# Performance work log

Hardware: AMD Instinct MI355X
Metric: run time of the kernel (lower is better)

Reference implementation:

```python
import math
import jax, jax.numpy as jnp
import numpy as np

B, S, HID = 2, 1024, 4096
NH, NKV, HD = 32, 8, 128
G = NH // NKV            # query heads per KV head (GQA group size)
PAST = 1024              # tokens already in the cache per sequence
L = PAST + S             # total KV tokens attended per sequence
SLOTS = 16384            # paged KV-cache slots (flat token addressing)
MAXPOS = 8192
THETA = 10000.0


def _rope_table():
    inv_freq = 1.0 / (THETA ** (np.arange(0, HD, 2, dtype=np.float64) / HD))
    freqs = np.arange(MAXPOS, dtype=np.float64)[:, None] * inv_freq[None, :]
    emb = np.concatenate([freqs, freqs], axis=-1)          # [MAXPOS, HD]
    return jnp.asarray(np.stack([np.cos(emb), np.sin(emb)], axis=1), jnp.float32)  # [MAXPOS,2,HD]


def setup_inputs() -> dict:
    key = jax.random.key(0)
    ks = jax.random.split(key, 6)
    hidden_states = jax.random.normal(ks[0], (B, S, HID), jnp.float32)
    kv_cache = jax.random.normal(ks[1], (SLOTS, 2, NKV, HD), jnp.float32)  # [slot, k/v, kv_head, hd]
    rope_cache = _rope_table()
    Wq = jax.random.normal(ks[2], (HID, NH * HD), jnp.float32) * 0.02
    Wk = jax.random.normal(ks[3], (HID, NKV * HD), jnp.float32) * 0.02
    Wv = jax.random.normal(ks[4], (HID, NKV * HD), jnp.float32) * 0.02
    Wo = jax.random.normal(ks[5], (NH * HD, HID), jnp.float32) * 0.02
    position_offsets = jnp.full((B,), PAST, jnp.int32)
    base = jnp.arange(B, dtype=jnp.int32)[:, None] * L            # each seq owns L contiguous slots
    kv_drain_addr_lut = base + PAST + jnp.arange(S, dtype=jnp.int32)[None, :]  # [B,S] write addrs
    kv_lut = base + jnp.arange(L, dtype=jnp.int32)[None, :]                    # [B,L] read addrs
    return {
        "hidden_states": hidden_states, "kv_cache": kv_cache, "rope_cache": rope_cache,
        "Wq": Wq, "Wk": Wk, "Wv": Wv, "Wo": Wo,
        "position_offsets": position_offsets,
        "kv_drain_addr_lut": kv_drain_addr_lut, "kv_lut": kv_lut,
    }


def _apply_rope(x, cos, sin):
    # x: [B, H, S, HD]; cos/sin: [B, 1, S, HD]
    x1, x2 = x[..., : HD // 2], x[..., HD // 2:]
    return x * cos + jnp.concatenate([-x2, x1], axis=-1) * sin


def reference(hidden_states, kv_cache, rope_cache, Wq, Wk, Wv, Wo,
              position_offsets, kv_drain_addr_lut, kv_lut):
    # QKV projections
    q = (hidden_states @ Wq).reshape(B, S, NH, HD).transpose(0, 2, 1, 3)    # [B,NH,S,HD]
    k = (hidden_states @ Wk).reshape(B, S, NKV, HD).transpose(0, 2, 1, 3)   # [B,NKV,S,HD]
    v = (hidden_states @ Wv).reshape(B, S, NKV, HD).transpose(0, 2, 1, 3)
    # RoPE at absolute positions
    pos = position_offsets[:, None] + jnp.arange(S, dtype=jnp.int32)        # [B,S]
    cos = rope_cache[pos, 0][:, None]                                       # [B,1,S,HD]
    sin = rope_cache[pos, 1][:, None]
    q = _apply_rope(q, cos, sin)
    k = _apply_rope(k, cos, sin)
    # LUT-addressed KV-cache drain (copy_kv_block)
    k_tok = k.transpose(0, 2, 1, 3).reshape(B * S, NKV, HD)
    v_tok = v.transpose(0, 2, 1, 3).reshape(B * S, NKV, HD)
    lut = kv_drain_addr_lut.reshape(-1)
    kv_cache = kv_cache.at[lut, 0].set(k_tok).at[lut, 1].set(v_tok)
    # Gather per-sequence KV pages and run grouped (GQA) causal attention
    kv = kv_cache[kv_lut]                                                   # [B,L,2,NKV,HD]
    keys = kv[:, :, 0].transpose(0, 2, 1, 3)                                # [B,NKV,L,HD]
    vals = kv[:, :, 1].transpose(0, 2, 1, 3)
    qg = q.reshape(B, NKV, G, S, HD)
    scores = jnp.einsum('bhgsd,bhld->bhgsl', qg, keys) * (HD ** -0.5)       # [B,NKV,G,S,L]
    kpos = jnp.arange(L, dtype=jnp.int32)
    causal = kpos[None, None, :] <= pos[:, :, None]                         # [B,S,L]
    scores = jnp.where(causal[:, None, None], scores, jnp.float32(-1e30))
    p = jax.nn.softmax(scores, axis=-1)
    out = jnp.einsum('bhgsl,bhld->bhgsd', p, vals).reshape(B, NH, S, HD)
    out = out.transpose(0, 2, 1, 3).reshape(B, S, HID)
    return out @ Wo
```

## Files before the change

### kernel.cpp

```cpp
#include <hip/hip_runtime.h>
#include <hip/hip_bf16.h>
#include <cstdint>
#include <cstddef>

#define B_    2
#define S_    1024
#define HID_  4096
#define NH_   32
#define NKV_  8
#define HD_   128
#define G_    4
#define PAST_ 1024
#define L_    2048
#define NQKV_ 6144

typedef __bf16 bf16_t;
typedef bf16_t bf16x4 __attribute__((ext_vector_type(4)));
typedef bf16_t bf16x8 __attribute__((ext_vector_type(8)));
typedef float  f32x4  __attribute__((ext_vector_type(4)));
typedef unsigned short ushort4_t __attribute__((ext_vector_type(4)));

__device__ __forceinline__ void gload_lds16(const bf16_t* g, bf16_t* l) {
  __builtin_amdgcn_global_load_lds(
      (const __attribute__((address_space(1))) void*)g,
      (__attribute__((address_space(3))) void*)l, 16, 0, 0);
}

__global__ __launch_bounds__(256) void cvt_bf16x8(const float* __restrict__ src,
                                                  bf16_t* __restrict__ dst) {
  size_t i = ((size_t)blockIdx.x * 256 + threadIdx.x) * 8;
  f32x4 a = *(const f32x4*)(src + i);
  f32x4 b = *(const f32x4*)(src + i + 4);
  bf16x8 o;
#pragma unroll
  for (int j = 0; j < 4; ++j) o[j] = (bf16_t)a[j];
#pragma unroll
  for (int j = 0; j < 4; ++j) o[4 + j] = (bf16_t)b[j];
  *(bf16x8*)(dst + i) = o;
}

__global__ __launch_bounds__(256) void wt_all(const float* __restrict__ Wq,
                                              const float* __restrict__ Wk,
                                              const float* __restrict__ Wv,
                                              const float* __restrict__ Wo,
                                              bf16_t* __restrict__ Wcat,
                                              bf16_t* __restrict__ Wot) {
  __shared__ float T[64][65];
  const int tid = threadIdx.x;
  const int bx = blockIdx.x;
  const float* src;
  bf16_t* dst;
  int C, c0;
  if (bx < 64)      { src = Wq; dst = Wcat;                         C = 4096; c0 = bx * 64; }
  else if (bx < 80) { src = Wk; dst = Wcat + (size_t)4096 * 4096;   C = 1024; c0 = (bx - 64) * 64; }
  else if (bx < 96) { src = Wv; dst = Wcat + (size_t)5120 * 4096;   C = 1024; c0 = (bx - 80) * 64; }
  else              { src = Wo; dst = Wot;                          C = 4096; c0 = (bx - 96) * 64; }
  const int r0 = blockIdx.y * 64;
  const int rr = tid >> 4;
  const int c4 = tid & 15;
#pragma unroll
  for (int i = 0; i < 4; ++i) {
    int row = i * 16 + rr;
    f32x4 v = *(const f32x4*)&src[(size_t)(r0 + row) * C + c0 + c4 * 4];
#pragma unroll
    for (int e = 0; e < 4; ++e) T[row][c4 * 4 + e] = v[e];
  }
  __syncthreads();
#pragma unroll
  for (int i = 0; i < 4; ++i) {
    int orow = i * 16 + rr;
    ushort4_t o;
#pragma unroll
    for (int e = 0; e < 4; ++e) {
      union { bf16_t b; unsigned short u; } cv;
      cv.b = (bf16_t)T[c4 * 4 + e][orow];
      o[e] = cv.u;
    }
    *(ushort4_t*)&dst[(size_t)(c0 + orow) * 4096 + r0 + c4 * 4] = o;
  }
}

template <int BN, bool OUT_BF16>
__global__ __launch_bounds__(512) void gemm8(const bf16_t* __restrict__ A,
                                             const bf16_t* __restrict__ Bt,
                                             void* __restrict__ C, int N, int K) {
  constexpr int BSLAB = BN * 32;
  constexpr int BUFE = 16384 + 2 * BSLAB;
  constexpr int NF = BN / 64;
  constexpr int WN = BN / 4;
  constexpr int BCH = BN * 4;
  __shared__ bf16_t sm[2 * BUFE];

  const int tid = threadIdx.x;
  const int lane = tid & 63;
  const int w = tid >> 6;
  const int wm = w >> 2, wn = w & 3;
  const int g = lane >> 4;
  const int r16 = lane & 15;

  const int flat = blockIdx.y * 32 + blockIdx.x;
  const int xcd = flat & 7;
  const int i2 = flat >> 3;
  const int tx = xcd * 4 + (i2 & 3);
  const int ty = i2 >> 2;
  const int m0 = ty * 256;
  const int n0 = tx * BN;

  const int NT = K >> 6;

  f32x4 acc[8][NF] = {};

  auto stageA = [&](int T, int j) {
    bf16_t* base = sm + (T & 1) * BUFE + j * 8192;
#pragma unroll
    for (int cj = 0; cj < 2; ++cj) {
      int c = (w * 2 + cj) * 64 + lane;
      int p = c * 16;
      int l = p ^ (((p >> 9) & 1) << 5);
      int row = l >> 6, colb = l & 63;
      gload_lds16(A + (size_t)(m0 + row) * K + T * 64 + j * 32 + (colb >> 1),
                  base + (w * 2 + cj) * 512);
    }
  };
  auto stageB = [&](int T, int j) {
    bf16_t* base = sm + (T & 1) * BUFE + 16384 + j * BSLAB;
#pragma unroll
    for (int cj = 0; cj < (BCH + 511) / 512; ++cj) {
      int cbase = cj * 512 + w * 64;
      if (cbase < BCH) {
        int c = cbase + lane;
        int p = c * 16;
        int l = p ^ (((p >> 9) & 1) << 5);
        int row = l >> 6, colb = l & 63;
        gload_lds16(Bt + (size_t)(n0 + row) * K + T * 64 + j * 32 + (colb >> 1),
                    base + cbase * 8);
      }
    }
  };

  stageA(0, 0); stageB(0, 0);
  stageA(0, 1); stageB(0, 1);
  __syncthreads();

#pragma unroll 2
  for (int T = 0; T < NT; ++T) {
    const bf16_t* abuf = sm + (T & 1) * BUFE;
    const bf16_t* bbuf = abuf + 16384;
#pragma unroll
    for (int j = 0; j < 2; ++j) {
      const bf16_t* as = abuf + j * 8192;
      const bf16_t* bs = bbuf + j * BSLAB;
      bf16x8 af[8];
      bf16x8 bfr[NF];
#pragma unroll
      for (int m = 0; m < 8; ++m) {
        int a = (wm * 128 + m * 16 + r16) * 64 + g * 16;
        a ^= ((a >> 9) & 1) << 5;
        af[m] = *(const bf16x8*)((const char*)as + a);
      }
#pragma unroll
      for (int n = 0; n < NF; ++n) {
        int a = (wn * WN + n * 16 + r16) * 64 + g * 16;
        a ^= ((a >> 9) & 1) << 5;
        bfr[n] = *(const bf16x8*)((const char*)bs + a);
      }
      if (j == 0 && T + 1 < NT) {
        stageA(T + 1, 0); stageB(T + 1, 0);
        stageA(T + 1, 1); stageB(T + 1, 1);
      }
      __builtin_amdgcn_s_setprio(1);
#pragma unroll
      for (int m = 0; m < 8; ++m)
#pragma unroll
        for (int n = 0; n < NF; ++n)
          acc[m][n] = __builtin_amdgcn_mfma_f32_16x16x32_bf16(af[m], bfr[n],
                                                              acc[m][n], 0, 0, 0);
      __builtin_amdgcn_s_setprio(0);
    }
    __syncthreads();
  }

#pragma unroll
  for (int m = 0; m < 8; ++m)
#pragma unroll
    for (int n = 0; n < NF; ++n)
#pragma unroll
      for (int r = 0; r < 4; ++r) {
        int row = m0 + wm * 128 + m * 16 + g * 4 + r;
        int col = n0 + wn * WN + n * 16 + r16;
        if (OUT_BF16)
          ((bf16_t*)C)[(size_t)row * N + col] = (bf16_t)acc[m][n][r];
        else
          ((float*)C)[(size_t)row * N + col] = acc[m][n][r];
      }
}

__global__ __launch_bounds__(256) void rope_pack(const bf16_t* __restrict__ QKV,
                                                 const float* __restrict__ rope,
                                                 bf16_t* __restrict__ Qb,
                                                 bf16_t* __restrict__ Kb) {
  const int tok = blockIdx.x;
  const int head = blockIdx.y * 2 + (threadIdx.x >> 7);
  const int d = threadIdx.x & 127;
  const int b = tok >> 10, s = tok & 1023;
  const int pos = PAST_ + s;
  const int off = head < NH_ ? head * HD_ : HID_ + (head - NH_) * HD_;
  const bf16_t* row = QKV + (size_t)tok * NQKV_;
  float x = (float)row[off + d];
  int dp = d < 64 ? d + 64 : d - 64;
  float xp = (float)row[off + dp];
  float c = rope[(size_t)(pos * 2) * HD_ + d];
  float sn = rope[(size_t)(pos * 2 + 1) * HD_ + d];
  float out = d < 64 ? x * c - xp * sn : x * c + xp * sn;
  if (head < NH_)
    Qb[((size_t)(b * NH_ + head) * S_ + s) * HD_ + d] = (bf16_t)out;
  else
    Kb[((size_t)(b * NKV_ + (head - NH_)) * L_ + PAST_ + s) * HD_ + d] = (bf16_t)out;
}

__global__ __launch_bounds__(256) void past_kv(const float* __restrict__ cache,
                                               const int* __restrict__ kv_lut,
                                               bf16_t* __restrict__ Kb,
                                               bf16_t* __restrict__ Vt) {
  __shared__ bf16_t Vs[128][72];
  const int tid = threadIdx.x;
  const int lt = blockIdx.x & 15;
  const int h = (blockIdx.x >> 4) & 7;
  const int b = blockIdx.x >> 7;
  const int l0 = lt * 64;
#pragma unroll
  for (int i = 0; i < 32; ++i) {
    int idx = i * 256 + tid;
    int l = idx >> 7, d = idx & 127;
    int slot = kv_lut[b * L_ + l0 + l];
    float kv = cache[((size_t)slot * 2 * NKV_ + h) * HD_ + d];
    float vv = cache[(((size_t)slot * 2 + 1) * NKV_ + h) * HD_ + d];
    Kb[((size_t)(b * NKV_ + h) * L_ + l0 + l) * HD_ + d] = (bf16_t)kv;
    Vs[d][l] = (bf16_t)vv;
  }
  __syncthreads();
#pragma unroll
  for (int i = 0; i < 32; ++i) {
    int idx = i * 256 + tid;
    int d = idx >> 6, l = idx & 63;
    Vt[((size_t)(b * NKV_ + h) * HD_ + d) * L_ + l0 + l] = Vs[d][l];
  }
}

__global__ __launch_bounds__(256) void v_pack(const bf16_t* __restrict__ QKV,
                                              bf16_t* __restrict__ Vt) {
  __shared__ bf16_t Vs[128][72];
  const int tid = threadIdx.x;
  const int st = blockIdx.x & 15;
  const int h = (blockIdx.x >> 4) & 7;
  const int b = blockIdx.x >> 7;
  const int s0 = st * 64;
#pragma unroll
  for (int i = 0; i < 32; ++i) {
    int idx = i * 256 + tid;
    int sl = idx >> 7, d = idx & 127;
    Vs[d][sl] = QKV[(size_t)(b * S_ + s0 + sl) * NQKV_ + HID_ + NKV_ * HD_ + h * HD_ + d];
  }
  __syncthreads();
#pragma unroll
  for (int i = 0; i < 32; ++i) {
    int idx = i * 256 + tid;
    int d = idx >> 6, l = idx & 63;
    Vt[((size_t)(b * NKV_ + h) * HD_ + d) * L_ + PAST_ + s0 + l] = Vs[d][l];
  }
}

__global__ __launch_bounds__(512) void attn(const bf16_t* __restrict__ Qb,
                                            const bf16_t* __restrict__ Kb,
                                            const bf16_t* __restrict__ Vt,
                                            bf16_t* __restrict__ Ctx) {
  __shared__ bf16_t smem[40960];

  const int tid = threadIdx.x;
  const int lane = tid & 63;
  const int w = tid >> 6;
  const int g = lane >> 4;
  const int r16 = lane & 15;
  const int rx = r16 & 7;

  const int id = blockIdx.x;
  const int kh = id & 7;
  const int b = (id >> 3) & 1;
  const int qh = (id >> 4) & 3;
  const int grp = id >> 6;
  const int qc = grp < 4 ? 7 - grp : grp - 4;
  const int h = kh * G_ + qh;

  const int s0w = qc * 128 + w * 16;

  const bf16_t* qp = Qb + ((size_t)(b * NH_ + h) * S_ + s0w + r16) * HD_ + g * 8;
  bf16x8 qf[4];
#pragma unroll
  for (int ks = 0; ks < 4; ++ks) qf[ks] = *(const bf16x8*)(qp + ks * 32);

  const bf16_t* kbase = Kb + (size_t)(b * NKV_ + kh) * L_ * HD_;
  const bf16_t* vbase = Vt + (size_t)(b * NKV_ + kh) * HD_ * L_;

  const int slot0 = w * 2;
  const int kl0 = slot0 * 4 + (lane >> 4);
  const int kc0 = (lane & 15) ^ (kl0 & 7);
  const int kl1 = kl0 + 4;
  const int kc1 = (lane & 15) ^ (kl1 & 7);
  const int vd0 = slot0 * 8 + (lane >> 3);
  const int vc0 = (lane & 7) ^ (vd0 & 7);
  const int vd1 = vd0 + 8;
  const int vc1 = (lane & 7) ^ (vd1 & 7);

  float m_run = -1e30f;
  float s_run = 0.f;
  f32x4 acc_o[8] = {};

  const float scale = 0.08838834764831845f;
  const int qpos_base = PAST_ + s0w;
  const int qpos = qpos_base + r16;
  const int nt_ = 18 + 2 * qc;

  {
    bf16_t* Kd = smem;
    bf16_t* Vd = smem + 16384;
    gload_lds16(kbase + (size_t)kl0 * HD_ + kc0 * 8, Kd + slot0 * 512);
    gload_lds16(kbase + (size_t)kl1 * HD_ + kc1 * 8, Kd + (slot0 + 1) * 512);
    gload_lds16(vbase + (size_t)vd0 * L_ + vc0 * 8, Vd + slot0 * 512);
    gload_lds16(vbase + (size_t)vd1 * L_ + vc1 * 8, Vd + (slot0 + 1) * 512);
  }
  __syncthreads();

  for (int t = 0; t < nt_; ++t) {
    const int cur = t & 1;
    const int lt = t * 64;

    if (t + 1 < nt_) {
      const int ltn = lt + 64;
      bf16_t* Kd = smem + (cur ^ 1) * 8192;
      bf16_t* Vd = smem + 16384 + (cur ^ 1) * 8192;
      gload_lds16(kbase + (size_t)(ltn + kl0) * HD_ + kc0 * 8, Kd + slot0 * 512);
      gload_lds16(kbase + (size_t)(ltn + kl1) * HD_ + kc1 * 8, Kd + (slot0 + 1) * 512);
      gload_lds16(vbase + (size_t)vd0 * L_ + ltn + vc0 * 8, Vd + slot0 * 512);
      gload_lds16(vbase + (size_t)vd1 * L_ + ltn + vc1 * 8, Vd + (slot0 + 1) * 512);
    }

    const bf16_t* Kc = smem + cur * 8192;
    const bf16_t* Vc = smem + 16384 + cur * 8192;
    bf16_t* Pw = smem + 32768 + w * 1024;

    f32x4 sc[4] = {};
#pragma unroll
    for (int nt = 0; nt < 4; ++nt) {
#pragma unroll
      for (int ks = 0; ks < 4; ++ks) {
        bf16x8 kf = *(const bf16x8*)&Kc[(nt * 16 + r16) * 128 + (((ks * 4 + g) ^ rx) << 3)];
        sc[nt] = __builtin_amdgcn_mfma_f32_16x16x32_bf16(kf, qf[ks], sc[nt], 0, 0, 0);
      }
    }

    const bool need_mask = (lt + 63) > qpos_base;
    float sv[4][4];
    float tmax = -1e30f;
#pragma unroll
    for (int nt = 0; nt < 4; ++nt)
#pragma unroll
      for (int r = 0; r < 4; ++r) {
        float v = sc[nt][r] * scale;
        if (need_mask) {
          int l = lt + nt * 16 + g * 4 + r;
          if (l > qpos) v = -1e30f;
        }
        sv[nt][r] = v;
        tmax = fmaxf(tmax, v);
      }
    tmax = fmaxf(tmax, __shfl_xor(tmax, 16, 64));
    tmax = fmaxf(tmax, __shfl_xor(tmax, 32, 64));

    if (!__all(tmax <= m_run + 8.f)) {
      float newm = fmaxf(m_run, tmax);
      float alpha = __expf(m_run - newm);
      m_run = newm;
      s_run *= alpha;
#pragma unroll
      for (int r = 0; r < 4; ++r) {
        float a = __shfl(alpha, g * 4 + r, 64);
#pragma unroll
        for (int d8 = 0; d8 < 8; ++d8) acc_o[d8][r] *= a;
      }
    }

    float psum = 0.f;
#pragma unroll
    for (int nt = 0; nt < 4; ++nt) {
      bf16x4 pk;
#pragma unroll
      for (int r = 0; r < 4; ++r) {
        float pv = __expf(sv[nt][r] - m_run);
        psum += pv;
        pk[r] = (bf16_t)pv;
      }
      *(bf16x4*)&Pw[r16 * 64 + (((nt * 2 + (g >> 1)) ^ rx) << 3) + (g & 1) * 4] = pk;
    }
    psum += __shfl_xor(psum, 16, 64);
    psum += __shfl_xor(psum, 32, 64);
    s_run += psum;

#pragma unroll
    for (int ks2 = 0; ks2 < 2; ++ks2) {
      bf16x8 pa = *(const bf16x8*)&Pw[r16 * 64 + (((ks2 * 4 + g) ^ rx) << 3)];
#pragma unroll
      for (int d8 = 0; d8 < 8; ++d8) {
        bf16x8 vf = *(const bf16x8*)&Vc[(d8 * 16 + r16) * 64 + (((ks2 * 4 + g) ^ rx) << 3)];
        acc_o[d8] = __builtin_amdgcn_mfma_f32_16x16x32_bf16(pa, vf, acc_o[d8], 0, 0, 0);
      }
    }

    __syncthreads();
  }

  float inv[4];
#pragma unroll
  for (int r = 0; r < 4; ++r) inv[r] = 1.f / __shfl(s_run, g * 4 + r, 64);
#pragma unroll
  for (int d8 = 0; d8 < 8; ++d8)
#pragma unroll
    for (int r = 0; r < 4; ++r) {
      int tok = b * S_ + s0w + g * 4 + r;
      int col = h * HD_ + d8 * 16 + r16;
      Ctx[(size_t)tok * HID_ + col] = (bf16_t)(acc_o[d8][r] * inv[r]);
    }
}

extern "C" void kernel_launch(void* const* d_in, const int* in_sizes, int n_in,
                              void* d_out, int out_size, void* d_ws, size_t ws_size,
                              hipStream_t stream) {
  const float* hidden = (const float*)d_in[0];
  const float* kv_cache = (const float*)d_in[1];
  const float* rope = (const float*)d_in[2];
  const float* Wq = (const float*)d_in[3];
  const float* Wk = (const float*)d_in[4];
  const float* Wv = (const float*)d_in[5];
  const float* Wo = (const float*)d_in[6];
  const int* kv_lut = (const int*)d_in[9];
  float* out = (float*)d_out;

  bf16_t* Xb = (bf16_t*)d_ws;
  bf16_t* Wcat = Xb + (size_t)2048 * 4096;
  bf16_t* Wot = Wcat + (size_t)6144 * 4096;
  bf16_t* QKVb = Wot + (size_t)4096 * 4096;
  bf16_t* Qb = QKVb + (size_t)2048 * 6144;
  bf16_t* Kb = Qb + (size_t)B_ * NH_ * S_ * HD_;
  bf16_t* Vt = Kb + (size_t)B_ * NKV_ * L_ * HD_;
  bf16_t* Ctx = Xb;

  cvt_bf16x8<<<4096, 256, 0, stream>>>(hidden, Xb);
  wt_all<<<dim3(160, 64), 256, 0, stream>>>(Wq, Wk, Wv, Wo, Wcat, Wot);

  gemm8<192, true><<<dim3(32, 8), 512, 0, stream>>>(Xb, Wcat, QKVb, NQKV_, HID_);

  rope_pack<<<dim3(2048, 20), 256, 0, stream>>>(QKVb, rope, Qb, Kb);
  past_kv<<<256, 256, 0, stream>>>(kv_cache, kv_lut, Kb, Vt);
  v_pack<<<256, 256, 0, stream>>>(QKVb, Vt);

  attn<<<512, 512, 0, stream>>>(Qb, Kb, Vt, Ctx);

  gemm8<128, false><<<dim3(32, 8), 512, 0, stream>>>(Ctx, Wot, out, HID_, HID_);
}
```

Before: 350.3 us.

## Process two 16-row query tiles per wave in attention, halving waves per block

After: 351.8 us. Within noise of the previous version (+0.4%).

```diff
diff --git a/kernel.cpp b/kernel.cpp
--- a/kernel.cpp
+++ b/kernel.cpp
@@ -270,10 +270,10 @@
   }
 }
 
-__global__ __launch_bounds__(512) void attn(const bf16_t* __restrict__ Qb,
-                                            const bf16_t* __restrict__ Kb,
-                                            const bf16_t* __restrict__ Vt,
-                                            bf16_t* __restrict__ Ctx) {
+__global__ __launch_bounds__(256, 2) void attn(const bf16_t* __restrict__ Qb,
+                                               const bf16_t* __restrict__ Kb,
+                                               const bf16_t* __restrict__ Vt,
+                                               bf16_t* __restrict__ Ctx) {
   __shared__ bf16_t smem[40960];
 
   const int tid = threadIdx.x;
@@ -293,141 +293,192 @@
 
   const int s0w = qc * 128 + w * 16;
 
-  const bf16_t* qp = Qb + ((size_t)(b * NH_ + h) * S_ + s0w + r16) * HD_ + g * 8;
-  bf16x8 qf[4];
-#pragma unroll
-  for (int ks = 0; ks < 4; ++ks) qf[ks] = *(const bf16x8*)(qp + ks * 32);
+  const bf16_t* qpA = Qb + ((size_t)(b * NH_ + h) * S_ + s0w + r16) * HD_ + g * 8;
+  const bf16_t* qpB = qpA + (size_t)64 * HD_;
+  bf16x8 qfA[4], qfB[4];
+#pragma unroll
+  for (int ks = 0; ks < 4; ++ks) {
+    qfA[ks] = *(const bf16x8*)(qpA + ks * 32);
+    qfB[ks] = *(const bf16x8*)(qpB + ks * 32);
+  }
 
   const bf16_t* kbase = Kb + (size_t)(b * NKV_ + kh) * L_ * HD_;
   const bf16_t* vbase = Vt + (size_t)(b * NKV_ + kh) * HD_ * L_;
 
-  const int slot0 = w * 2;
-  const int kl0 = slot0 * 4 + (lane >> 4);
-  const int kc0 = (lane & 15) ^ (kl0 & 7);
-  const int kl1 = kl0 + 4;
-  const int kc1 = (lane & 15) ^ (kl1 & 7);
-  const int vd0 = slot0 * 8 + (lane >> 3);
-  const int vc0 = (lane & 7) ^ (vd0 & 7);
-  const int vd1 = vd0 + 8;
-  const int vc1 = (lane & 7) ^ (vd1 & 7);
-
-  float m_run = -1e30f;
-  float s_run = 0.f;
-  f32x4 acc_o[8] = {};
+  float mA = -1e30f, mB = -1e30f;
+  float sA = 0.f, sB = 0.f;
+  f32x4 accA[8] = {}, accB[8] = {};
 
   const float scale = 0.08838834764831845f;
-  const int qpos_base = PAST_ + s0w;
-  const int qpos = qpos_base + r16;
+  const int qbaseA = PAST_ + s0w;
+  const int qbaseB = qbaseA + 64;
+  const int qposA = qbaseA + r16;
+  const int qposB = qbaseB + r16;
   const int nt_ = 18 + 2 * qc;
 
-  {
-    bf16_t* Kd = smem;
-    bf16_t* Vd = smem + 16384;
-    gload_lds16(kbase + (size_t)kl0 * HD_ + kc0 * 8, Kd + slot0 * 512);
-    gload_lds16(kbase + (size_t)kl1 * HD_ + kc1 * 8, Kd + (slot0 + 1) * 512);
-    gload_lds16(vbase + (size_t)vd0 * L_ + vc0 * 8, Vd + slot0 * 512);
-    gload_lds16(vbase + (size_t)vd1 * L_ + vc1 * 8, Vd + (slot0 + 1) * 512);
-  }
+  auto stage = [&](int buf, int lt) {
+    bf16_t* Kd = smem + buf * 8192;
+    bf16_t* Vd = smem + 16384 + buf * 8192;
+#pragma unroll
+    for (int cj = 0; cj < 4; ++cj) {
+      int slot = w * 4 + cj;
+      int kl = slot * 4 + (lane >> 4);
+      int kc = (lane & 15) ^ (kl & 7);
+      gload_lds16(kbase + (size_t)(lt + kl) * HD_ + kc * 8, Kd + slot * 512);
+      int vd = slot * 8 + (lane >> 3);
+      int vc = (lane & 7) ^ (vd & 7);
+      gload_lds16(vbase + (size_t)vd * L_ + lt + vc * 8, Vd + slot * 512);
+    }
+  };
+
+  stage(0, 0);
   __syncthreads();
 
   for (int t = 0; t < nt_; ++t) {
     const int cur = t & 1;
     const int lt = t * 64;
 
-    if (t + 1 < nt_) {
-      const int ltn = lt + 64;
-      bf16_t* Kd = smem + (cur ^ 1) * 8192;
-      bf16_t* Vd = smem + 16384 + (cur ^ 1) * 8192;
-      gload_lds16(kbase + (size_t)(ltn + kl0) * HD_ + kc0 * 8, Kd + slot0 * 512);
-      gload_lds16(kbase + (size_t)(ltn + kl1) * HD_ + kc1 * 8, Kd + (slot0 + 1) * 512);
-      gload_lds16(vbase + (size_t)vd0 * L_ + ltn + vc0 * 8, Vd + slot0 * 512);
-      gload_lds16(vbase + (size_t)vd1 * L_ + ltn + vc1 * 8, Vd + (slot0 + 1) * 512);
-    }
+    if (t + 1 < nt_) stage(cur ^ 1, lt + 64);
 
     const bf16_t* Kc = smem + cur * 8192;
     const bf16_t* Vc = smem + 16384 + cur * 8192;
-    bf16_t* Pw = smem + 32768 + w * 1024;
-
-    f32x4 sc[4] = {};
+    bf16_t* PwA = smem + 32768 + w * 2048;
+    bf16_t* PwB = PwA + 1024;
+
+    f32x4 scA[4] = {}, scB[4] = {};
 #pragma unroll
     for (int nt = 0; nt < 4; ++nt) {
 #pragma unroll
       for (int ks = 0; ks < 4; ++ks) {
         bf16x8 kf = *(const bf16x8*)&Kc[(nt * 16 + r16) * 128 + (((ks * 4 + g) ^ rx) << 3)];
-        sc[nt] = __builtin_amdgcn_mfma_f32_16x16x32_bf16(kf, qf[ks], sc[nt], 0, 0, 0);
-      }
-    }
-
-    const bool need_mask = (lt + 63) > qpos_base;
-    float sv[4][4];
-    float tmax = -1e30f;
-#pragma unroll
-    for (int nt = 0; nt < 4; ++nt)
-#pragma unroll
-      for (int r = 0; r < 4; ++r) {
-        float v = sc[nt][r] * scale;
-        if (need_mask) {
-          int l = lt + nt * 16 + g * 4 + r;
-          if (l > qpos) v = -1e30f;
+        scA[nt] = __builtin_amdgcn_mfma_f32_16x16x32_bf16(kf, qfA[ks], scA[nt], 0, 0, 0);
+        scB[nt] = __builtin_amdgcn_mfma_f32_16x16x32_bf16(kf, qfB[ks], scB[nt], 0, 0, 0);
+      }
+    }
+
+    {
+      const bool need_mask = (lt + 63) > qbaseA;
+      float sv[4][4];
+      float tmax = -1e30f;
+#pragma unroll
+      for (int nt = 0; nt < 4; ++nt)
+#pragma unroll
+        for (int r = 0; r < 4; ++r) {
+          float v = scA[nt][r] * scale;
+          if (need_mask) {
+            int l = lt + nt * 16 + g * 4 + r;
+            if (l > qposA) v = -1e30f;
+          }
+          sv[nt][r] = v;
+          tmax = fmaxf(tmax, v);
         }
-        sv[nt][r] = v;
-        tmax = fmaxf(tmax, v);
-      }
-    tmax = fmaxf(tmax, __shfl_xor(tmax, 16, 64));
-    tmax = fmaxf(tmax, __shfl_xor(tmax, 32, 64));
-
-    if (!__all(tmax <= m_run + 8.f)) {
-      float newm = fmaxf(m_run, tmax);
-      float alpha = __expf(m_run - newm);
-      m_run = newm;
-      s_run *= alpha;
-#pragma unroll
-      for (int r = 0; r < 4; ++r) {
-        float a = __shfl(alpha, g * 4 + r, 64);
-#pragma unroll
-        for (int d8 = 0; d8 < 8; ++d8) acc_o[d8][r] *= a;
-      }
-    }
-
-    float psum = 0.f;
-#pragma unroll
-    for (int nt = 0; nt < 4; ++nt) {
-      bf16x4 pk;
-#pragma unroll
-      for (int r = 0; r < 4; ++r) {
-        float pv = __expf(sv[nt][r] - m_run);
-        psum += pv;
-        pk[r] = (bf16_t)pv;
-      }
-      *(bf16x4*)&Pw[r16 * 64 + (((nt * 2 + (g >> 1)) ^ rx) << 3) + (g & 1) * 4] = pk;
-    }
-    psum += __shfl_xor(psum, 16, 64);
-    psum += __shfl_xor(psum, 32, 64);
-    s_run += psum;
+      tmax = fmaxf(tmax, __shfl_xor(tmax, 16, 64));
+      tmax = fmaxf(tmax, __shfl_xor(tmax, 32, 64));
+      if (!__all(tmax <= mA + 8.f)) {
+        float newm = fmaxf(mA, tmax);
+        float alpha = __expf(mA - newm);
+        mA = newm;
+        sA *= alpha;
+#pragma unroll
+        for (int r = 0; r < 4; ++r) {
+          float a = __shfl(alpha, g * 4 + r, 64);
+#pragma unroll
+          for (int d8 = 0; d8 < 8; ++d8) accA[d8][r] *= a;
+        }
+      }
+      float psum = 0.f;
+#pragma unroll
+      for (int nt = 0; nt < 4; ++nt) {
+        bf16x4 pk;
+#pragma unroll
+        for (int r = 0; r < 4; ++r) {
+          float pv = __expf(sv[nt][r] - mA);
+          psum += pv;
+          pk[r] = (bf16_t)pv;
+        }
+        *(bf16x4*)&PwA[r16 * 64 + (((nt * 2 + (g >> 1)) ^ rx) << 3) + (g & 1) * 4] = pk;
+      }
+      psum += __shfl_xor(psum, 16, 64);
+      psum += __shfl_xor(psum, 32, 64);
+      sA += psum;
+    }
+
+    {
+      const bool need_mask = (lt + 63) > qbaseB;
+      float sv[4][4];
+      float tmax = -1e30f;
+#pragma unroll
+      for (int nt = 0; nt < 4; ++nt)
+#pragma unroll
+        for (int r = 0; r < 4; ++r) {
+          float v = scB[nt][r] * scale;
+          if (need_mask) {
+            int l = lt + nt * 16 + g * 4 + r;
+            if (l > qposB) v = -1e30f;
+          }
+          sv[nt][r] = v;
+          tmax = fmaxf(tmax, v);
+        }
+      tmax = fmaxf(tmax, __shfl_xor(tmax, 16, 64));
+      tmax = fmaxf(tmax, __shfl_xor(tmax, 32, 64));
+      if (!__all(tmax <= mB + 8.f)) {
+        float newm = fmaxf(mB, tmax);
+        float alpha = __expf(mB - newm);
+        mB = newm;
+        sB *= alpha;
+#pragma unroll
+        for (int r = 0; r < 4; ++r) {
+          float a = __shfl(alpha, g * 4 + r, 64);
+#pragma unroll
+          for (int d8 = 0; d8 < 8; ++d8) accB[d8][r] *= a;
+        }
+      }
+      float psum = 0.f;
+#pragma unroll
+      for (int nt = 0; nt < 4; ++nt) {
+        bf16x4 pk;
+#pragma unroll
+        for (int r = 0; r < 4; ++r) {
+          float pv = __expf(sv[nt][r] - mB);
+          psum += pv;
+          pk[r] = (bf16_t)pv;
+        }
+        *(bf16x4*)&PwB[r16 * 64 + (((nt * 2 + (g >> 1)) ^ rx) << 3) + (g & 1) * 4] = pk;
+      }
+      psum += __shfl_xor(psum, 16, 64);
+      psum += __shfl_xor(psum, 32, 64);
+      sB += psum;
+    }
 
 #pragma unroll
     for (int ks2 = 0; ks2 < 2; ++ks2) {
-      bf16x8 pa = *(const bf16x8*)&Pw[r16 * 64 + (((ks2 * 4 + g) ^ rx) << 3)];
+      bf16x8 paA = *(const bf16x8*)&PwA[r16 * 64 + (((ks2 * 4 + g) ^ rx) << 3)];
+      bf16x8 paB = *(const bf16x8*)&PwB[r16 * 64 + (((ks2 * 4 + g) ^ rx) << 3)];
 #pragma unroll
       for (int d8 = 0; d8 < 8; ++d8) {
         bf16x8 vf = *(const bf16x8*)&Vc[(d8 * 16 + r16) * 64 + (((ks2 * 4 + g) ^ rx) << 3)];
-        acc_o[d8] = __builtin_amdgcn_mfma_f32_16x16x32_bf16(pa, vf, acc_o[d8], 0, 0, 0);
+        accA[d8] = __builtin_amdgcn_mfma_f32_16x16x32_bf16(paA, vf, accA[d8], 0, 0, 0);
+        accB[d8] = __builtin_amdgcn_mfma_f32_16x16x32_bf16(paB, vf, accB[d8], 0, 0, 0);
       }
     }
 
     __syncthreads();
   }
 
-  float inv[4];
-#pragma unroll
-  for (int r = 0; r < 4; ++r) inv[r] = 1.f / __shfl(s_run, g * 4 + r, 64);
+  float invA[4], invB[4];
+#pragma unroll
+  for (int r = 0; r < 4; ++r) {
+    invA[r] = 1.f / __shfl(sA, g * 4 + r, 64);
+    invB[r] = 1.f / __shfl(sB, g * 4 + r, 64);
+  }
 #pragma unroll
   for (int d8 = 0; d8 < 8; ++d8)
 #pragma unroll
     for (int r = 0; r < 4; ++r) {
-      int tok = b * S_ + s0w + g * 4 + r;
+      int tokA = b * S_ + s0w + g * 4 + r;
       int col = h * HD_ + d8 * 16 + r16;
-      Ctx[(size_t)tok * HID_ + col] = (bf16_t)(acc_o[d8][r] * inv[r]);
+      Ctx[(size_t)tokA * HID_ + col] = (bf16_t)(accA[d8][r] * invA[r]);
+      Ctx[(size_t)(tokA + 64) * HID_ + col] = (bf16_t)(accB[d8][r] * invB[r]);
     }
 }
 
@@ -462,7 +513,7 @@
   past_kv<<<256, 256, 0, stream>>>(kv_cache, kv_lut, Kb, Vt);
   v_pack<<<256, 256, 0, stream>>>(QKVb, Vt);
 
-  attn<<<512, 512, 0, stream>>>(Qb, Kb, Vt, Ctx);
+  attn<<<512, 256, 0, stream>>>(Qb, Kb, Vt, Ctx);
 
   gemm8<128, false><<<dim3(32, 8), 512, 0, stream>>>(Ctx, Wot, out, HID_, HID_);
 }
```
